# Kernel tuning notes

Hardware: AMD Instinct MI355X
Metric: run time of the kernel (lower is better)

## Reference

```python
import jax, jax.numpy as jnp
import numpy as np

N = 100_000      # num nodes
E = 6_400_000    # num edges
P = 12           # periods
F = 32           # output_size (TGCN hidden)


def setup_inputs() -> dict:
    key = jax.random.key(0)
    ks = jax.random.split(key, 16)
    g = lambda i, shape, s=0.1: jax.random.normal(ks[i], shape, dtype=jnp.float32) * s
    zf = jnp.zeros((F,), jnp.float32)
    return {
        "x": jax.random.normal(ks[0], (N, P), dtype=jnp.float32),
        "edge_index": jax.random.randint(ks[1], (2, E), 0, N, dtype=jnp.int64),
        "edge_weight": jax.random.uniform(ks[2], (E,), dtype=jnp.float32),
        "attention": g(3, (P,), 1.0),            # A3TGCN learned period attention
        # GCNConv weights: in_channels=1 -> weight is effectively a length-F vector
        "wc_z": g(4, (F,)), "bc_z": zf,
        "wc_r": g(5, (F,)), "bc_r": zf,
        "wc_h": g(6, (F,)), "bc_h": zf,
        # TGCN gate linears: Linear(2F, F) with bias
        "wl_z": g(7, (2 * F, F)), "bl_z": zf,
        "wl_r": g(8, (2 * F, F)), "bl_r": zf,
        "wl_h": g(9, (2 * F, F)), "bl_h": zf,
        # final Linear(F, 1)
        "w_out": g(10, (F, 1)), "b_out": jnp.zeros((1,), jnp.float32),
    }


def reference(x, edge_index, edge_weight, attention,
              wc_z, bc_z, wc_r, bc_r, wc_h, bc_h,
              wl_z, bl_z, wl_r, bl_r, wl_h, bl_h,
              w_out, b_out):
    n = x.shape[0]
    src, dst = edge_index[0], edge_index[1]

    # GCN normalization with added self-loops (weight 1): D^{-1/2} (A + I) D^{-1/2}
    deg = jax.ops.segment_sum(edge_weight, dst, num_segments=n) + 1.0
    dinv = jax.lax.rsqrt(deg)
    norm = dinv[src] * edge_weight * dinv[dst]          # (E,)

    # GCNConv is linear and in_channels == 1, so conv_g(X_p)_i = agg(X_p)_i * W_g + b_g
    # where agg is the normalized (self-loop augmented) scalar aggregation.
    # Aggregate all periods at once: (E, P) messages -> (N, P)
    agg = jax.ops.segment_sum(norm[:, None] * x[src], dst, num_segments=n)
    agg = agg + (dinv * dinv)[:, None] * x              # self-loop term, (N, P)

    probs = jax.nn.softmax(attention)                   # (P,)
    H0 = jnp.zeros((n, F), x.dtype)                     # A3TGCN calls TGCN with H=None each period
    H_acc = jnp.zeros((n, F), x.dtype)
    for p in range(P):                                  # small fixed structural loop
        s = agg[:, p, None]                             # (N, 1)
        conv_z = s * wc_z + bc_z                        # (N, F)
        conv_r = s * wc_r + bc_r
        conv_h = s * wc_h + bc_h
        Z = jax.nn.sigmoid(jnp.concatenate([conv_z, H0], axis=1) @ wl_z + bl_z)
        R = jax.nn.sigmoid(jnp.concatenate([conv_r, H0], axis=1) @ wl_r + bl_r)
        Ht = jnp.tanh(jnp.concatenate([conv_h, H0 * R], axis=1) @ wl_h + bl_h)
        Hp = Z * H0 + (1.0 - Z) * Ht                    # TGCN single step from zero state
        H_acc = H_acc + probs[p] * Hp

    h = jax.nn.relu(H_acc)
    return h @ w_out + b_out                            # (N, 1)
```

## Files before the change

kernel.cpp:

```cpp
#include <hip/hip_runtime.h>

#define NN 100000
#define EE 6400000
#define PP 12
#define FF 32

#define VV    128
#define BB    782
#define K1B   800
#define CHK   8000
#define NBIN  784
#define XST   16
#define K1SEG 400
#define CAP2  4576
#define NR2   9
#define FPSI  (1.0f / 4294967296.0f)

__global__ void precompute_k(const float* __restrict__ att,
                             const float* __restrict__ wc_z, const float* __restrict__ bc_z,
                             const float* __restrict__ wc_h, const float* __restrict__ bc_h,
                             const float* __restrict__ wl_z, const float* __restrict__ bl_z,
                             const float* __restrict__ wl_h, const float* __restrict__ bl_h,
                             float* __restrict__ tabs) {
    int j = threadIdx.x;
    if (j < FF) {
        float az = 0.f, cz = 0.f, ah = 0.f, ch = 0.f;
        for (int f = 0; f < FF; ++f) {
            float wz = wl_z[f * FF + j];
            float wh = wl_h[f * FF + j];
            az += wc_z[f] * wz;
            cz += bc_z[f] * wz;
            ah += wc_h[f] * wh;
            ch += bc_h[f] * wh;
        }
        tabs[16 + j]          = az;
        tabs[16 + FF + j]     = cz + bl_z[j];
        tabs[16 + 2 * FF + j] = ah;
        tabs[16 + 3 * FF + j] = ch + bl_h[j];
    } else if (j == FF) {
        float a[PP];
        float m = -1e30f;
        for (int p = 0; p < PP; ++p) { a[p] = att[p]; m = fmaxf(m, a[p]); }
        float s = 0.f;
        for (int p = 0; p < PP; ++p) { a[p] = __expf(a[p] - m); s += a[p]; }
        for (int p = 0; p < PP; ++p) tabs[p] = a[p] / s;
    }
}

__global__ __launch_bounds__(512) void bucketsort_k(const int* __restrict__ src,
                                                    const int* __restrict__ dst,
                                                    const float* __restrict__ ew,
                                                    uint2* __restrict__ recs,
                                                    unsigned short* __restrict__ T16) {
    __shared__ unsigned int perm[CHK];
    __shared__ int hist[NBIN];
    __shared__ int offs[NBIN];
    int tid = threadIdx.x;
    int blk = blockIdx.x;
    int beg = blk * CHK;

    for (int b = tid; b < NBIN; b += 512) hist[b] = 0;
    __syncthreads();

    for (int e = tid; e < CHK; e += 512)
        atomicAdd(&hist[dst[beg + e] >> 7], 1);
    __syncthreads();

    int i2   = 512 + tid;
    int own0 = hist[tid];
    int own1 = (i2 < NBIN) ? hist[i2] : 0;
    for (int off = 1; off < NBIN; off <<= 1) {
        int a0 = (tid >= off) ? hist[tid - off] : 0;
        int a1 = (i2 < NBIN) ? hist[i2 - off] : 0;
        __syncthreads();
        hist[tid] += a0;
        if (i2 < NBIN) hist[i2] += a1;
        __syncthreads();
    }
    offs[tid] = hist[tid] - own0;
    if (i2 < NBIN) offs[i2] = hist[i2] - own1;
    __syncthreads();

    for (int b = tid; b < BB + 1; b += 512)
        T16[(size_t)b * K1B + blk] = (unsigned short)offs[b];
    __syncthreads();

    for (int e = tid; e < CHK; e += 512) {
        int d = dst[beg + e];
        int p = atomicAdd(&offs[d >> 7], 1);
        perm[p] = ((unsigned)(d & (VV - 1)) << 13) | (unsigned)e;
    }
    __syncthreads();

    uint2* o = recs + (size_t)blk * CHK;
    for (int k = tid; k < CHK; k += 512) {
        unsigned pe = perm[k];
        int e = (int)(pe & 0x1FFFu);
        uint2 r;
        r.x = ((pe >> 13) << 17) | (unsigned)src[beg + e];
        r.y = __float_as_uint(ew[beg + e]);
        o[k] = r;
    }
}

__global__ __launch_bounds__(512) void deg2_k(const uint2* __restrict__ recs,
                                              const unsigned short* __restrict__ T16,
                                              unsigned long long* __restrict__ pdeg) {
    __shared__ unsigned long long wsum[VV];
    __shared__ unsigned short rstart[K1SEG];
    __shared__ int rpre[K1SEG + 1];
    int b   = blockIdx.x >> 1;
    int seg = blockIdx.x & 1;
    int tid = threadIdx.x;
    int k0  = seg * K1SEG;

    if (tid < VV) wsum[tid] = 0ull;
    if (tid < K1SEG) {
        int s = T16[(size_t)b * K1B + k0 + tid];
        int e = T16[(size_t)(b + 1) * K1B + k0 + tid];
        rstart[tid] = (unsigned short)s;
        rpre[tid]   = e - s;
    }
    __syncthreads();

    for (int off = 1; off < K1SEG; off <<= 1) {
        int a = (tid < K1SEG && tid >= off) ? rpre[tid - off] : 0;
        __syncthreads();
        if (tid < K1SEG) rpre[tid] += a;
        __syncthreads();
    }
    int inc = (tid < K1SEG) ? rpre[tid] : 0;
    __syncthreads();
    if (tid == 0) rpre[0] = 0;
    if (tid < K1SEG) rpre[tid + 1] = inc;
    __syncthreads();

    int n = rpre[K1SEG];
    for (int k = tid; k < n; k += 512) {
        int r = 0;
        #pragma unroll
        for (int s = 256; s; s >>= 1) {
            int c = r + s;
            if (c < K1SEG && rpre[c] <= k) r = c;
        }
        uint2 v = recs[(size_t)(k0 + r) * CHK + rstart[r] + (k - rpre[r])];
        unsigned long long w = (unsigned long long)(__uint_as_float(v.y) * 4294967296.0f);
        atomicAdd(&wsum[v.x >> 17], w);
    }
    __syncthreads();

    int node = b * VV + tid;
    if (tid < VV && node < NN)
        pdeg[(size_t)seg * NN + node] = wsum[tid];
}

__global__ __launch_bounds__(256) void xds_k(const unsigned long long* __restrict__ pdeg,
                                             const float* __restrict__ x,
                                             float* __restrict__ xds) {
    int i = blockIdx.x * 256 + threadIdx.x;
    if (i >= NN) return;
    float wf = (float)(pdeg[i] + pdeg[(size_t)NN + i]) * FPSI;
    float dv = rsqrtf(wf + 1.0f);
    const float4* xr = (const float4*)(x + (size_t)i * PP);
    float4* xo = (float4*)(xds + ((size_t)i << 4));
    #pragma unroll
    for (int q = 0; q < 3; ++q) {
        float4 v = xr[q];
        v.x *= dv; v.y *= dv; v.z *= dv; v.w *= dv;
        xo[q] = v;
    }
    xds[((size_t)i << 4) + 12] = dv;
}

__global__ __launch_bounds__(512) void sortagg_k(const uint2* __restrict__ recs,
                                                 const unsigned short* __restrict__ T16,
                                                 const float* __restrict__ xds,
                                                 float* __restrict__ pagg) {
    __shared__ uint2 srec[CAP2];
    __shared__ int   h[VV], starts_s[VV], offs[VV];
    __shared__ unsigned short rstart[K1SEG];
    __shared__ int   rpre[K1SEG + 1];
    int b   = blockIdx.x >> 1;
    int seg = blockIdx.x & 1;
    int tid = threadIdx.x;
    int k0  = seg * K1SEG;

    if (tid < VV) h[tid] = 0;
    if (tid < K1SEG) {
        int s = T16[(size_t)b * K1B + k0 + tid];
        int e = T16[(size_t)(b + 1) * K1B + k0 + tid];
        rstart[tid] = (unsigned short)s;
        rpre[tid]   = e - s;
    }
    __syncthreads();

    for (int off = 1; off < K1SEG; off <<= 1) {
        int a = (tid < K1SEG && tid >= off) ? rpre[tid - off] : 0;
        __syncthreads();
        if (tid < K1SEG) rpre[tid] += a;
        __syncthreads();
    }
    int inc = (tid < K1SEG) ? rpre[tid] : 0;
    __syncthreads();
    if (tid == 0) rpre[0] = 0;
    if (tid < K1SEG) rpre[tid + 1] = inc;
    __syncthreads();

    int n = min(rpre[K1SEG], 512 * NR2);

    uint2 regs[NR2];
    #pragma unroll
    for (int w = 0; w < NR2; ++w) {
        int k = tid + w * 512;
        if (k < n) {
            int r = 0;
            #pragma unroll
            for (int s = 256; s; s >>= 1) {
                int c = r + s;
                if (c < K1SEG && rpre[c] <= k) r = c;
            }
            uint2 v = recs[(size_t)(k0 + r) * CHK + rstart[r] + (k - rpre[r])];
            regs[w] = v;
            atomicAdd(&h[v.x >> 17], 1);
        }
    }
    __syncthreads();

    int own = (tid < VV) ? h[tid] : 0;
    #pragma unroll
    for (int off = 1; off < VV; off <<= 1) {
        int t = (tid < VV && tid >= off) ? h[tid - off] : 0;
        __syncthreads();
        if (tid < VV) h[tid] += t;
        __syncthreads();
    }
    if (tid < VV) {
        int pre = h[tid] - own;
        starts_s[tid] = pre;
        offs[tid]     = pre;
    }
    __syncthreads();

    #pragma unroll
    for (int w = 0; w < NR2; ++w) {
        int k = tid + w * 512;
        if (k < n) {
            uint2 v = regs[w];
            int p = atomicAdd(&offs[v.x >> 17], 1);
            if (p < CAP2) srec[p] = v;
        }
    }
    __syncthreads();

    int local = tid >> 2;
    int q     = tid & 3;
    int st = min(starts_s[local], CAP2);
    int en = min(h[local], CAP2);

    float acc[PP];
    #pragma unroll
    for (int p = 0; p < PP; ++p) acc[p] = 0.f;

    for (int m = st + q; m < en; m += 4) {
        uint2 v = srec[m];
        float c = __uint_as_float(v.y);
        const float4* xs = (const float4*)(xds + ((size_t)(v.x & 0x1FFFFu) << 4));
        float4 v0 = xs[0], v1 = xs[1], v2 = xs[2];
        acc[0] += c * v0.x;  acc[1] += c * v0.y;  acc[2]  += c * v0.z;  acc[3]  += c * v0.w;
        acc[4] += c * v1.x;  acc[5] += c * v1.y;  acc[6]  += c * v1.z;  acc[7]  += c * v1.w;
        acc[8] += c * v2.x;  acc[9] += c * v2.y;  acc[10] += c * v2.z;  acc[11] += c * v2.w;
    }

    #pragma unroll
    for (int p = 0; p < PP; ++p) {
        acc[p] += __shfl_xor(acc[p], 1, 4);
        acc[p] += __shfl_xor(acc[p], 2, 4);
    }

    float* ap = pagg + ((size_t)(seg * BB + b) * VV + local) * PP;
    ap[3 * q + 0] = acc[3 * q + 0];
    ap[3 * q + 1] = acc[3 * q + 1];
    ap[3 * q + 2] = acc[3 * q + 2];
}

__global__ __launch_bounds__(512) void epi_k(const float* __restrict__ pagg,
                                             const float* __restrict__ xds,
                                             const float* __restrict__ tabs,
                                             const float* __restrict__ w_out,
                                             const float* __restrict__ b_out,
                                             float* __restrict__ out) {
    int b = blockIdx.x;
    int tid = threadIdx.x;
    int g = tid >> 5;
    int j = tid & 31;
    float azj = tabs[16 + j];
    float czj = tabs[16 + FF + j];
    float ahj = tabs[16 + 2 * FF + j];
    float chj = tabs[16 + 3 * FF + j];

    for (int nl = g; nl < VV; nl += 16) {
        int i = b * VV + nl;
        if (i >= NN) continue;
        float dv = xds[((size_t)i << 4) + 12];
        const float* a0 = pagg + ((size_t)b * VV + nl) * PP;
        const float* a1 = pagg + ((size_t)(BB + b) * VV + nl) * PP;

        float accum = 0.f;
        #pragma unroll
        for (int p = 0; p < PP; ++p) {
            float ai = a0[p] + a1[p];
            float sp = dv * (ai + xds[((size_t)i << 4) + p]);
            float pr = tabs[p];
            float uz = sp * azj + czj;
            float uh = sp * ahj + chj;
            float one_minus_z = 1.0f / (1.0f + __expf(uz));
            float e2h = __expf(2.0f * uh);
            float th  = 1.0f - 2.0f / (e2h + 1.0f);
            accum += pr * one_minus_z * th;
        }
        float hv = fmaxf(accum, 0.f) * w_out[j];
        #pragma unroll
        for (int off = 16; off > 0; off >>= 1)
            hv += __shfl_xor(hv, off, 32);
        if (j == 0) out[i] = hv + b_out[0];
    }
}

__global__ __launch_bounds__(256) void deg_k(const int* __restrict__ dst,
                                             const float* __restrict__ ew,
                                             float* __restrict__ deg) {
    int stride = gridDim.x * blockDim.x;
    for (int e = blockIdx.x * blockDim.x + threadIdx.x; e < EE; e += stride)
        atomicAdd(&deg[dst[e]], ew[e]);
}

__global__ __launch_bounds__(256) void dinv_self_k(const float* __restrict__ x,
                                                   float* __restrict__ deg,
                                                   float* __restrict__ agg) {
    int i = blockIdx.x * blockDim.x + threadIdx.x;
    if (i >= NN) return;
    float d  = deg[i] + 1.0f;
    float dv = rsqrtf(d);
    deg[i]   = dv;
    float dv2 = dv * dv;
    const float4* xr = (const float4*)(x + (size_t)i * PP);
    float4* ar = (float4*)(agg + (size_t)i * PP);
    #pragma unroll
    for (int q = 0; q < 3; ++q) {
        float4 v = xr[q];
        v.x *= dv2; v.y *= dv2; v.z *= dv2; v.w *= dv2;
        ar[q] = v;
    }
}

__global__ __launch_bounds__(256) void agg_k(const int* __restrict__ src,
                                             const int* __restrict__ dst,
                                             const float* __restrict__ ew,
                                             const float* __restrict__ x,
                                             const float* __restrict__ dinv,
                                             float* __restrict__ agg) {
    int stride = gridDim.x * blockDim.x;
    for (int e = blockIdx.x * blockDim.x + threadIdx.x; e < EE; e += stride) {
        int s = src[e];
        int d = dst[e];
        float nw = dinv[s] * ew[e] * dinv[d];
        const float4* xs = (const float4*)(x + (size_t)s * PP);
        float* ad = agg + (size_t)d * PP;
        float4 v0 = xs[0], v1 = xs[1], v2 = xs[2];
        atomicAdd(&ad[0],  nw * v0.x);
        atomicAdd(&ad[1],  nw * v0.y);
        atomicAdd(&ad[2],  nw * v0.z);
        atomicAdd(&ad[3],  nw * v0.w);
        atomicAdd(&ad[4],  nw * v1.x);
        atomicAdd(&ad[5],  nw * v1.y);
        atomicAdd(&ad[6],  nw * v1.z);
        atomicAdd(&ad[7],  nw * v1.w);
        atomicAdd(&ad[8],  nw * v2.x);
        atomicAdd(&ad[9],  nw * v2.y);
        atomicAdd(&ad[10], nw * v2.z);
        atomicAdd(&ad[11], nw * v2.w);
    }
}

__global__ __launch_bounds__(256) void node_k(const float* __restrict__ agg,
                                              const float* __restrict__ tabs,
                                              const float* __restrict__ w_out,
                                              const float* __restrict__ b_out,
                                              float* __restrict__ out) {
    int t = blockIdx.x * blockDim.x + threadIdx.x;
    int i = t >> 5;
    int j = t & 31;
    if (i >= NN) return;
    float azj = tabs[16 + j];
    float czj = tabs[16 + FF + j];
    float ahj = tabs[16 + 2 * FF + j];
    float chj = tabs[16 + 3 * FF + j];
    float acc = 0.f;
    #pragma unroll
    for (int p = 0; p < PP; ++p) {
        float s  = agg[i * PP + p];
        float pr = tabs[p];
        float uz = s * azj + czj;
        float uh = s * ahj + chj;
        float one_minus_z = 1.0f / (1.0f + __expf(uz));
        float e2h = __expf(2.0f * uh);
        float th  = 1.0f - 2.0f / (e2h + 1.0f);
        acc += pr * one_minus_z * th;
    }
    float h = fmaxf(acc, 0.f) * w_out[j];
    #pragma unroll
    for (int off = 16; off > 0; off >>= 1)
        h += __shfl_xor(h, off, 32);
    if (j == 0) out[i] = h + b_out[0];
}

extern "C" void kernel_launch(void* const* d_in, const int* in_sizes, int n_in,
                              void* d_out, int out_size, void* d_ws, size_t ws_size,
                              hipStream_t stream) {
    const float* x    = (const float*)d_in[0];
    const int*   ei   = (const int*)d_in[1];
    const float* ew   = (const float*)d_in[2];
    const float* att  = (const float*)d_in[3];
    const float* wc_z = (const float*)d_in[4];
    const float* bc_z = (const float*)d_in[5];
    const float* wc_h = (const float*)d_in[8];
    const float* bc_h = (const float*)d_in[9];
    const float* wl_z = (const float*)d_in[10];
    const float* bl_z = (const float*)d_in[11];
    const float* wl_h = (const float*)d_in[14];
    const float* bl_h = (const float*)d_in[15];
    const float* wout = (const float*)d_in[16];
    const float* bout = (const float*)d_in[17];
    float* out = (float*)d_out;

    const int* src = ei;
    const int* dst = ei + EE;

    size_t region  = (size_t)EE * sizeof(uint2);
    size_t tbl_sz  = (((size_t)(BB + 1) * K1B * 2) + 63) & ~63ull;
    size_t xds_sz  = (size_t)NN * XST * sizeof(float);
    size_t pdeg_sz = (size_t)2 * NN * sizeof(unsigned long long);
    size_t pagg_sz = (size_t)2 * BB * VV * PP * sizeof(float);
    size_t need    = region + tbl_sz + xds_sz + pdeg_sz + pagg_sz + 4096;

    if (ws_size >= need) {
        char* base = (char*)d_ws;
        uint2*              recs = (uint2*)base;                 base += region;
        unsigned short*     T16  = (unsigned short*)base;        base += tbl_sz;
        float*              xds  = (float*)base;                 base += xds_sz;
        unsigned long long* pdeg = (unsigned long long*)base;    base += pdeg_sz;
        float*              pagg = (float*)base;                 base += pagg_sz;
        float*              tabs = (float*)base;

        precompute_k<<<1, 64, 0, stream>>>(att, wc_z, bc_z, wc_h, bc_h, wl_z, bl_z, wl_h, bl_h, tabs);
        bucketsort_k<<<K1B, 512, 0, stream>>>(src, dst, ew, recs, T16);
        deg2_k<<<BB * 2, 512, 0, stream>>>(recs, T16, pdeg);
        xds_k<<<(NN + 255) / 256, 256, 0, stream>>>(pdeg, x, xds);
        sortagg_k<<<BB * 2, 512, 0, stream>>>(recs, T16, xds, pagg);
        epi_k<<<BB, 512, 0, stream>>>(pagg, xds, tabs, wout, bout, out);
    } else {
        float* deg  = (float*)d_ws;
        float* agg  = deg + NN;
        float* tabs = agg + (size_t)NN * PP;

        hipMemsetAsync(deg, 0, NN * sizeof(float), stream);
        precompute_k<<<1, 64, 0, stream>>>(att, wc_z, bc_z, wc_h, bc_h, wl_z, bl_z, wl_h, bl_h, tabs);
        deg_k<<<4096, 256, 0, stream>>>(dst, ew, deg);
        dinv_self_k<<<(NN + 255) / 256, 256, 0, stream>>>(x, deg, agg);
        agg_k<<<8192, 256, 0, stream>>>(src, dst, ew, x, deg, agg);
        node_k<<<NN * 32 / 256, 256, 0, stream>>>(agg, tabs, wout, bout, out);
    }
}
```

Measured before the change: 362.0 us.

## Compute degree via global 64-bit atomics and split aggregation into four segments

Result: slower. 617.6 us (+70.6%).

```diff
diff --git a/kernel.cpp b/kernel.cpp
--- a/kernel.cpp
+++ b/kernel.cpp
@@ -11,9 +11,11 @@
 #define CHK   8000
 #define NBIN  784
 #define XST   16
-#define K1SEG 400
-#define CAP2  4576
-#define NR2   9
+#define NSEG  4
+#define K1SEG 200
+#define CAP2  2432
+#define NR2   5
+#define FPS   4294967296.0f
 #define FPSI  (1.0f / 4294967296.0f)
 
 __global__ void precompute_k(const float* __restrict__ att,
@@ -47,6 +49,32 @@
     }
 }
 
+__global__ __launch_bounds__(256) void deg64_k(const int* __restrict__ dst,
+                                               const float* __restrict__ ew,
+                                               unsigned long long* __restrict__ deg64) {
+    int stride = gridDim.x * blockDim.x;
+    for (int e = blockIdx.x * blockDim.x + threadIdx.x; e < EE; e += stride)
+        atomicAdd(&deg64[dst[e]], (unsigned long long)(long long)(ew[e] * FPS));
+}
+
+__global__ __launch_bounds__(256) void xds_k(const unsigned long long* __restrict__ deg64,
+                                             const float* __restrict__ x,
+                                             float* __restrict__ xds) {
+    int i = blockIdx.x * 256 + threadIdx.x;
+    if (i >= NN) return;
+    float wf = (float)deg64[i] * FPSI;
+    float dv = rsqrtf(wf + 1.0f);
+    const float4* xr = (const float4*)(x + (size_t)i * PP);
+    float4* xo = (float4*)(xds + ((size_t)i << 4));
+    #pragma unroll
+    for (int q = 0; q < 3; ++q) {
+        float4 v = xr[q];
+        v.x *= dv; v.y *= dv; v.z *= dv; v.w *= dv;
+        xo[q] = v;
+    }
+    xds[((size_t)i << 4) + 12] = dv;
+}
+
 __global__ __launch_bounds__(512) void bucketsort_k(const int* __restrict__ src,
                                                     const int* __restrict__ dst,
                                                     const float* __restrict__ ew,
@@ -103,75 +131,6 @@
     }
 }
 
-__global__ __launch_bounds__(512) void deg2_k(const uint2* __restrict__ recs,
-                                              const unsigned short* __restrict__ T16,
-                                              unsigned long long* __restrict__ pdeg) {
-    __shared__ unsigned long long wsum[VV];
-    __shared__ unsigned short rstart[K1SEG];
-    __shared__ int rpre[K1SEG + 1];
-    int b   = blockIdx.x >> 1;
-    int seg = blockIdx.x & 1;
-    int tid = threadIdx.x;
-    int k0  = seg * K1SEG;
-
-    if (tid < VV) wsum[tid] = 0ull;
-    if (tid < K1SEG) {
-        int s = T16[(size_t)b * K1B + k0 + tid];
-        int e = T16[(size_t)(b + 1) * K1B + k0 + tid];
-        rstart[tid] = (unsigned short)s;
-        rpre[tid]   = e - s;
-    }
-    __syncthreads();
-
-    for (int off = 1; off < K1SEG; off <<= 1) {
-        int a = (tid < K1SEG && tid >= off) ? rpre[tid - off] : 0;
-        __syncthreads();
-        if (tid < K1SEG) rpre[tid] += a;
-        __syncthreads();
-    }
-    int inc = (tid < K1SEG) ? rpre[tid] : 0;
-    __syncthreads();
-    if (tid == 0) rpre[0] = 0;
-    if (tid < K1SEG) rpre[tid + 1] = inc;
-    __syncthreads();
-
-    int n = rpre[K1SEG];
-    for (int k = tid; k < n; k += 512) {
-        int r = 0;
-        #pragma unroll
-        for (int s = 256; s; s >>= 1) {
-            int c = r + s;
-            if (c < K1SEG && rpre[c] <= k) r = c;
-        }
-        uint2 v = recs[(size_t)(k0 + r) * CHK + rstart[r] + (k - rpre[r])];
-        unsigned long long w = (unsigned long long)(__uint_as_float(v.y) * 4294967296.0f);
-        atomicAdd(&wsum[v.x >> 17], w);
-    }
-    __syncthreads();
-
-    int node = b * VV + tid;
-    if (tid < VV && node < NN)
-        pdeg[(size_t)seg * NN + node] = wsum[tid];
-}
-
-__global__ __launch_bounds__(256) void xds_k(const unsigned long long* __restrict__ pdeg,
-                                             const float* __restrict__ x,
-                                             float* __restrict__ xds) {
-    int i = blockIdx.x * 256 + threadIdx.x;
-    if (i >= NN) return;
-    float wf = (float)(pdeg[i] + pdeg[(size_t)NN + i]) * FPSI;
-    float dv = rsqrtf(wf + 1.0f);
-    const float4* xr = (const float4*)(x + (size_t)i * PP);
-    float4* xo = (float4*)(xds + ((size_t)i << 4));
-    #pragma unroll
-    for (int q = 0; q < 3; ++q) {
-        float4 v = xr[q];
-        v.x *= dv; v.y *= dv; v.z *= dv; v.w *= dv;
-        xo[q] = v;
-    }
-    xds[((size_t)i << 4) + 12] = dv;
-}
-
 __global__ __launch_bounds__(512) void sortagg_k(const uint2* __restrict__ recs,
                                                  const unsigned short* __restrict__ T16,
                                                  const float* __restrict__ xds,
@@ -180,8 +139,8 @@
     __shared__ int   h[VV], starts_s[VV], offs[VV];
     __shared__ unsigned short rstart[K1SEG];
     __shared__ int   rpre[K1SEG + 1];
-    int b   = blockIdx.x >> 1;
-    int seg = blockIdx.x & 1;
+    int b   = blockIdx.x >> 2;
+    int seg = blockIdx.x & 3;
     int tid = threadIdx.x;
     int k0  = seg * K1SEG;
 
@@ -215,7 +174,7 @@
         if (k < n) {
             int r = 0;
             #pragma unroll
-            for (int s = 256; s; s >>= 1) {
+            for (int s = 128; s; s >>= 1) {
                 int c = r + s;
                 if (c < K1SEG && rpre[c] <= k) r = c;
             }
@@ -303,12 +262,14 @@
         if (i >= NN) continue;
         float dv = xds[((size_t)i << 4) + 12];
         const float* a0 = pagg + ((size_t)b * VV + nl) * PP;
-        const float* a1 = pagg + ((size_t)(BB + b) * VV + nl) * PP;
+        const float* a1 = a0 + (size_t)BB * VV * PP;
+        const float* a2 = a1 + (size_t)BB * VV * PP;
+        const float* a3 = a2 + (size_t)BB * VV * PP;
 
         float accum = 0.f;
         #pragma unroll
         for (int p = 0; p < PP; ++p) {
-            float ai = a0[p] + a1[p];
+            float ai = (a0[p] + a1[p]) + (a2[p] + a3[p]);
             float sp = dv * (ai + xds[((size_t)i << 4) + p]);
             float pr = tabs[p];
             float uz = sp * azj + czj;
@@ -439,24 +400,25 @@
     size_t region  = (size_t)EE * sizeof(uint2);
     size_t tbl_sz  = (((size_t)(BB + 1) * K1B * 2) + 63) & ~63ull;
     size_t xds_sz  = (size_t)NN * XST * sizeof(float);
-    size_t pdeg_sz = (size_t)2 * NN * sizeof(unsigned long long);
-    size_t pagg_sz = (size_t)2 * BB * VV * PP * sizeof(float);
-    size_t need    = region + tbl_sz + xds_sz + pdeg_sz + pagg_sz + 4096;
+    size_t deg_sz  = (size_t)NN * sizeof(unsigned long long);
+    size_t pagg_sz = (size_t)NSEG * BB * VV * PP * sizeof(float);
+    size_t need    = region + tbl_sz + xds_sz + deg_sz + pagg_sz + 4096;
 
     if (ws_size >= need) {
         char* base = (char*)d_ws;
-        uint2*              recs = (uint2*)base;                 base += region;
-        unsigned short*     T16  = (unsigned short*)base;        base += tbl_sz;
-        float*              xds  = (float*)base;                 base += xds_sz;
-        unsigned long long* pdeg = (unsigned long long*)base;    base += pdeg_sz;
-        float*              pagg = (float*)base;                 base += pagg_sz;
-        float*              tabs = (float*)base;
-
+        uint2*              recs  = (uint2*)base;               base += region;
+        unsigned short*     T16   = (unsigned short*)base;      base += tbl_sz;
+        float*              xds   = (float*)base;               base += xds_sz;
+        unsigned long long* deg64 = (unsigned long long*)base;  base += deg_sz;
+        float*              pagg  = (float*)base;               base += pagg_sz;
+        float*              tabs  = (float*)base;
+
+        hipMemsetAsync(deg64, 0, deg_sz, stream);
         precompute_k<<<1, 64, 0, stream>>>(att, wc_z, bc_z, wc_h, bc_h, wl_z, bl_z, wl_h, bl_h, tabs);
+        deg64_k<<<4096, 256, 0, stream>>>(dst, ew, deg64);
+        xds_k<<<(NN + 255) / 256, 256, 0, stream>>>(deg64, x, xds);
         bucketsort_k<<<K1B, 512, 0, stream>>>(src, dst, ew, recs, T16);
-        deg2_k<<<BB * 2, 512, 0, stream>>>(recs, T16, pdeg);
-        xds_k<<<(NN + 255) / 256, 256, 0, stream>>>(pdeg, x, xds);
-        sortagg_k<<<BB * 2, 512, 0, stream>>>(recs, T16, xds, pagg);
+        sortagg_k<<<BB * NSEG, 512, 0, stream>>>(recs, T16, xds, pagg);
         epi_k<<<BB, 512, 0, stream>>>(pagg, xds, tabs, wout, bout, out);
     } else {
         float* deg  = (float*)d_ws;
```
